# Kernel tuning notes

Measured on AMD Instinct MI355X. Metric: run time of the kernel, lower is better.

## Reference

```python
import jax, jax.numpy as jnp
import numpy as np

B, N, D = 32, 512, 256          # batch, instances, node_input_dim
M_DIM = 64                       # metric embedding dim
HID = 256                        # hidden_dim
COUNTS_PATTERN = [8, 16, 32, 72] # ragged per-instance metric counts (avg 32)


def _build_segments():
    counts = np.tile(np.array(COUNTS_PATTERN, dtype=np.int64), N // len(COUNTS_PATTERN))
    # metric_to_instance[t] = index of instance owning metric row t (contiguous ragged segments)
    return jnp.asarray(np.repeat(np.arange(N, dtype=np.int64), counts))


def setup_inputs() -> dict:
    key = jax.random.key(0)
    ks = jax.random.split(key, 8)
    metric_to_instance = _build_segments()
    T = int(metric_to_instance.shape[0])  # total_metrics = 16384
    h_instances = jax.random.normal(ks[0], (B, N, D), dtype=jnp.float32)
    metric_embeddings = jax.random.normal(ks[1], (B, T, M_DIM), dtype=jnp.float32)
    s = 0.02
    W1 = jax.random.normal(ks[2], (D + M_DIM, HID), dtype=jnp.float32) * s
    b1 = jnp.zeros((HID,), dtype=jnp.float32)
    W2 = jax.random.normal(ks[3], (HID, HID // 2), dtype=jnp.float32) * s
    b2 = jnp.zeros((HID // 2,), dtype=jnp.float32)
    W3 = jax.random.normal(ks[4], (HID // 2, 1), dtype=jnp.float32) * s
    b3 = jnp.zeros((1,), dtype=jnp.float32)
    return {
        "h_instances": h_instances,
        "metric_embeddings": metric_embeddings,
        "metric_to_instance": metric_to_instance,
        "W1": W1, "b1": b1, "W2": W2, "b2": b2, "W3": W3, "b3": b3,
    }


def reference(h_instances, metric_embeddings, metric_to_instance, W1, b1, W2, b2, W3, b3):
    # Gather each metric row's owning instance feature: [B, T, D]
    inst = jnp.take(h_instances, metric_to_instance, axis=1)
    # Concat with metric embedding -> [B, T, D + M_DIM]
    x = jnp.concatenate([inst, metric_embeddings], axis=-1)
    # metric_predictor MLP (Dropout is eval-mode identity in torch forward at inference)
    h = jax.nn.relu(jnp.einsum("btk,kh->bth", x, W1) + b1)
    h = jax.nn.relu(jnp.einsum("bth,hm->btm", h, W2) + b2)
    out = jnp.einsum("btm,mo->bto", h, W3) + b3  # [B, T, 1]
    return out[..., 0]  # [B, total_metrics]
```

## Files before the change

### kernel.cpp

```cpp
#include <hip/hip_runtime.h>

typedef _Float16 f16;
typedef f16  f16x2 __attribute__((ext_vector_type(2)));
typedef f16  f16x8 __attribute__((ext_vector_type(8)));
typedef float f32x16 __attribute__((ext_vector_type(16)));
typedef unsigned int u32;

#define MFMA32 __builtin_amdgcn_mfma_f32_32x32x16_f16

static __device__ __forceinline__ f16x8 cvt8(float4 a, float4 b) {
    f16x8 v;
    v[0]=(f16)a.x; v[1]=(f16)a.y; v[2]=(f16)a.z; v[3]=(f16)a.w;
    v[4]=(f16)b.x; v[5]=(f16)b.y; v[6]=(f16)b.z; v[7]=(f16)b.w;
    return v;
}
static __device__ __forceinline__ u32 pack2(float a, float b) {
    f16x2 p; p[0]=(f16)a; p[1]=(f16)b;
    return __builtin_bit_cast(u32, p);
}
static __device__ __forceinline__ u32 pk_add(u32 a, u32 b) {
    u32 d; asm("v_pk_add_f16 %0, %1, %2" : "=v"(d) : "v"(a), "v"(b)); return d;
}
static __device__ __forceinline__ u32 pk_relu(u32 a) {
    u32 d; asm("v_pk_max_f16 %0, %1, 0" : "=v"(d) : "v"(a)); return d;
}

__global__ __launch_bounds__(256) void prepack(
    const float* __restrict__ W1, const float* __restrict__ W2,
    f16* __restrict__ pa, f16* __restrict__ pb, f16* __restrict__ pc)
{
    const int idx = blockIdx.x * 256 + threadIdx.x;
    int rel, fid, mt, ks;
    const int lane = (idx >> 3) & 63;
    const int j    = idx & 7;
    const int g8   = ((lane >> 5) << 3) + j;
    const int ln   = lane & 31;
    if (idx < 65536) {
        rel = idx; fid = rel >> 9; mt = fid >> 4; ks = fid & 15;
        int k = 16 * ks + g8, col = 32 * mt + ln;
        pa[rel] = (f16)W1[k * 256 + col];
    } else if (idx < 81920) {
        rel = idx - 65536; fid = rel >> 9; mt = fid >> 2; ks = fid & 3;
        int k = 16 * ks + g8, col = 32 * mt + ln;
        pb[rel] = (f16)W1[(256 + k) * 256 + col];
    } else {
        rel = idx - 81920; fid = rel >> 9; mt = fid >> 4; ks = fid & 15;
        int k = 16 * ks + g8, col = 32 * mt + ln;
        pc[rel] = (f16)W2[k * 128 + col];
    }
}

__global__ __launch_bounds__(256) void ainit(
    const float* __restrict__ H,
    const f16x8* __restrict__ pW1a,
    const float* __restrict__ B1,
    f16* __restrict__ Af)
{
    const int tid = threadIdx.x, wid = tid >> 6, lane = tid & 63;
    const int g = lane >> 5, ln = lane & 31;
    const long ir = (long)blockIdx.x * 32 + ln;

    const float4* h4 = (const float4*)(H + ir * 256);
    f16x8 hf[16];
    #pragma unroll
    for (int ks = 0; ks < 16; ++ks)
        hf[ks] = cvt8(h4[4 * ks + 2 * g], h4[4 * ks + 2 * g + 1]);

    const float4* b14 = (const float4*)B1;
    #pragma unroll
    for (int mi = 0; mi < 2; ++mi) {
        const int mt = wid * 2 + mi;
        f32x16 acc;
        #pragma unroll
        for (int q = 0; q < 4; ++q) {
            float4 bv = b14[8 * mt + 2 * q + g];
            acc[4*q+0] = bv.x; acc[4*q+1] = bv.y; acc[4*q+2] = bv.z; acc[4*q+3] = bv.w;
        }
        #pragma unroll
        for (int ks = 0; ks < 16; ++ks)
            acc = MFMA32(pW1a[(mt * 16 + ks) * 64 + lane], hf[ks], acc, 0, 0, 0);
        #pragma unroll
        for (int q = 0; q < 4; ++q) {
            uint2 w;
            w.x = pack2(acc[4*q+0], acc[4*q+1]);
            w.y = pack2(acc[4*q+2], acc[4*q+3]);
            ((uint2*)Af)[ir * 64 + g * 32 + mt * 4 + q] = w;
        }
    }
}

__global__ __launch_bounds__(768, 3) void fused_mlp(
    const float* __restrict__ ME,
    const int*   __restrict__ SEG,
    const f16*   __restrict__ Af,
    const f16x8* __restrict__ pW1b,
    const f16x8* __restrict__ pW2,
    const float* __restrict__ B2,
    const float* __restrict__ W3,
    const float* __restrict__ B3,
    float* __restrict__ OUT)
{
    __shared__ f16x8 sW1b[2048];
    __shared__ f16x8 sW2[4096];
    const int tid = threadIdx.x, wid = tid >> 6, lane = tid & 63;
    const int g = lane >> 5, ln = lane & 31;

    for (int i = tid; i < 2048; i += 768) sW1b[i] = pW1b[i];
    for (int i = tid; i < 4096; i += 768) sW2[i]  = pW2[i];
    __syncthreads();

    const int bswz  = ((int)blockIdx.x & 7) * 32 + ((int)blockIdx.x >> 3);
    const int gwave = bswz * 12 + wid;

    const uint4* AB = (const uint4*)Af;
    const float4* b24 = (const float4*)B2;
    const float4* w34 = (const float4*)W3;
    const float  b3v  = B3[0];

    int tile = gwave;
    int ar_cur = ((tile >> 9) << 9) + SEG[((tile & 511) << 5) + ln];
    uint4 Av[4];
    #pragma unroll
    for (int u = 0; u < 4; ++u) Av[u] = AB[(long)ar_cur * 32 + g * 16 + u];

    while (true) {
        const int next = tile + 3072;
        int ar_nxt = ar_cur;
        if (next < 16384)
            ar_nxt = ((next >> 9) << 9) + SEG[((next & 511) << 5) + ln];

        const long row_base = (long)tile << 5;

        const float4* mb = (const float4*)(ME + (row_base + ln) * 64);
        float4 m0 = mb[2*g],     m1 = mb[2*g + 1];
        float4 m2_ = mb[4 + 2*g], m3 = mb[4 + 2*g + 1];
        float4 m4 = mb[8 + 2*g], m5 = mb[8 + 2*g + 1];
        float4 m6 = mb[12 + 2*g], m7 = mb[12 + 2*g + 1];
        f16x8 mef[4];
        mef[0] = cvt8(m0, m1); mef[1] = cvt8(m2_, m3);
        mef[2] = cvt8(m4, m5); mef[3] = cvt8(m6, m7);

        f32x16 acc2[4];
        #pragma unroll
        for (int m2 = 0; m2 < 4; ++m2)
            #pragma unroll
            for (int i = 0; i < 16; ++i) acc2[m2][i] = 0.f;

        #pragma unroll
        for (int mt = 0; mt < 8; ++mt) {
            const int sl = (mt & 1) * 2;
            const uint4 a0 = Av[sl], a1 = Av[sl + 1];
            {
                const int pos = mt + 2;
                if (pos < 8) {
                    Av[sl]     = AB[(long)ar_cur * 32 + g * 16 + 2*pos];
                    Av[sl + 1] = AB[(long)ar_cur * 32 + g * 16 + 2*pos + 1];
                } else if (next < 16384) {
                    const int mtn = pos - 8;
                    Av[sl]     = AB[(long)ar_nxt * 32 + g * 16 + 2*mtn];
                    Av[sl + 1] = AB[(long)ar_nxt * 32 + g * 16 + 2*mtn + 1];
                }
            }

            f32x16 acc;
            #pragma unroll
            for (int i = 0; i < 16; ++i) acc[i] = 0.f;
            #pragma unroll
            for (int s = 0; s < 4; ++s)
                acc = MFMA32(sW1b[(mt * 4 + s) * 64 + lane], mef[s], acc, 0, 0, 0);

            u32 hpt[8];
            hpt[0] = pk_relu(pk_add(pack2(acc[0],  acc[1]),  a0.x));
            hpt[1] = pk_relu(pk_add(pack2(acc[2],  acc[3]),  a0.y));
            hpt[2] = pk_relu(pk_add(pack2(acc[4],  acc[5]),  a0.z));
            hpt[3] = pk_relu(pk_add(pack2(acc[6],  acc[7]),  a0.w));
            hpt[4] = pk_relu(pk_add(pack2(acc[8],  acc[9]),  a1.x));
            hpt[5] = pk_relu(pk_add(pack2(acc[10], acc[11]), a1.y));
            hpt[6] = pk_relu(pk_add(pack2(acc[12], acc[13]), a1.z));
            hpt[7] = pk_relu(pk_add(pack2(acc[14], acc[15]), a1.w));

            #pragma unroll
            for (int tt = 0; tt < 2; ++tt) {
                u32 w0 = hpt[4*tt+0], w1 = hpt[4*tt+1];
                u32 w2 = hpt[4*tt+2], w3 = hpt[4*tt+3];
                asm("v_permlane32_swap_b32 %0, %1" : "+v"(w0), "+v"(w2));
                asm("v_permlane32_swap_b32 %0, %1" : "+v"(w1), "+v"(w3));
                int wv[4] = {(int)w0, (int)w1, (int)w2, (int)w3};
                f16x8 bf;
                __builtin_memcpy(&bf, wv, 16);
                const int ks2 = 2 * mt + tt;
                __builtin_amdgcn_s_setprio(1);
                #pragma unroll
                for (int m2 = 0; m2 < 4; ++m2)
                    acc2[m2] = MFMA32(sW2[(m2 * 16 + ks2) * 64 + lane], bf, acc2[m2], 0, 0, 0);
                __builtin_amdgcn_s_setprio(0);
            }
        }

        float sum = 0.f;
        #pragma unroll
        for (int m2 = 0; m2 < 4; ++m2)
            #pragma unroll
            for (int q = 0; q < 4; ++q) {
                float4 bb = b24[8*m2 + 2*q + g];
                float4 ww = w34[8*m2 + 2*q + g];
                sum += fmaxf(acc2[m2][4*q+0] + bb.x, 0.f) * ww.x
                     + fmaxf(acc2[m2][4*q+1] + bb.y, 0.f) * ww.y
                     + fmaxf(acc2[m2][4*q+2] + bb.z, 0.f) * ww.z
                     + fmaxf(acc2[m2][4*q+3] + bb.w, 0.f) * ww.w;
            }
        sum += __shfl_xor(sum, 32, 64);
        if (lane < 32) OUT[row_base + ln] = sum + b3v;

        if (next >= 16384) break;
        tile = next;
        ar_cur = ar_nxt;
    }
}

extern "C" void kernel_launch(void* const* d_in, const int* in_sizes, int n_in,
                              void* d_out, int out_size, void* d_ws, size_t ws_size,
                              hipStream_t stream) {
    const float* h_inst = (const float*)d_in[0];
    const float* me     = (const float*)d_in[1];
    const int*   seg    = (const int*)d_in[2];
    const float* W1     = (const float*)d_in[3];
    const float* b1     = (const float*)d_in[4];
    const float* W2     = (const float*)d_in[5];
    const float* b2     = (const float*)d_in[6];
    const float* W3     = (const float*)d_in[7];
    const float* b3     = (const float*)d_in[8];
    float* out = (float*)d_out;

    char* ws = (char*)d_ws;
    f16* Af   = (f16*)ws;
    f16* pW1a = (f16*)(ws + 8388608);
    f16* pW1b = (f16*)(ws + 8388608 + 131072);
    f16* pW2  = (f16*)(ws + 8388608 + 131072 + 32768);

    prepack<<<448, 256, 0, stream>>>(W1, W2, pW1a, pW1b, pW2);
    ainit<<<512, 256, 0, stream>>>(h_inst, (const f16x8*)pW1a, b1, Af);
    fused_mlp<<<256, 768, 0, stream>>>(me, seg, Af, (const f16x8*)pW1b,
                                       (const f16x8*)pW2, b2, W3, b3, out);
}
```

Baseline: 94.97 us.

## Replace static tile striding with atomic work-stealing counter in fused MLP

Each wave now claims its next 32-row tile through a global atomic counter, which prepack resets, instead of walking a fixed swizzled stride of 3072 tiles. This is meant to even out load imbalance across waves and CUs. The cross-tile prefetch of the next tile's A rows is dropped: A loads now start at the top of each tile, and only the segment index is prefetched. In exchange the kernel pays one atomic per tile per wave and exposes more latency on the A loads.

Measured after the change: 258.7 us. 2.72x slower.

```diff
diff --git a/kernel.cpp b/kernel.cpp
--- a/kernel.cpp
+++ b/kernel.cpp
@@ -27,8 +27,10 @@
 
 __global__ __launch_bounds__(256) void prepack(
     const float* __restrict__ W1, const float* __restrict__ W2,
-    f16* __restrict__ pa, f16* __restrict__ pb, f16* __restrict__ pc)
+    f16* __restrict__ pa, f16* __restrict__ pb, f16* __restrict__ pc,
+    int* __restrict__ ctr)
 {
+    if (blockIdx.x == 0 && threadIdx.x == 0) *ctr = 0;
     const int idx = blockIdx.x * 256 + threadIdx.x;
     int rel, fid, mt, ks;
     const int lane = (idx >> 3) & 63;
@@ -98,47 +100,51 @@
     const float* __restrict__ B2,
     const float* __restrict__ W3,
     const float* __restrict__ B3,
+    int* __restrict__ ctr,
     float* __restrict__ OUT)
 {
     __shared__ f16x8 sW1b[2048];
     __shared__ f16x8 sW2[4096];
-    const int tid = threadIdx.x, wid = tid >> 6, lane = tid & 63;
+    const int tid = threadIdx.x, lane = tid & 63;
     const int g = lane >> 5, ln = lane & 31;
 
     for (int i = tid; i < 2048; i += 768) sW1b[i] = pW1b[i];
     for (int i = tid; i < 4096; i += 768) sW2[i]  = pW2[i];
     __syncthreads();
-
-    const int bswz  = ((int)blockIdx.x & 7) * 32 + ((int)blockIdx.x >> 3);
-    const int gwave = bswz * 12 + wid;
 
     const uint4* AB = (const uint4*)Af;
     const float4* b24 = (const float4*)B2;
     const float4* w34 = (const float4*)W3;
     const float  b3v  = B3[0];
 
-    int tile = gwave;
-    int ar_cur = ((tile >> 9) << 9) + SEG[((tile & 511) << 5) + ln];
-    uint4 Av[4];
-    #pragma unroll
-    for (int u = 0; u < 4; ++u) Av[u] = AB[(long)ar_cur * 32 + g * 16 + u];
+    int cur;
+    if (lane == 0) cur = atomicAdd(ctr, 1);
+    cur = __builtin_amdgcn_readfirstlane(cur);
+    if (cur >= 16384) return;
+    int sv_cur = SEG[((cur & 511) << 5) + ln];
 
     while (true) {
-        const int next = tile + 3072;
-        int ar_nxt = ar_cur;
-        if (next < 16384)
-            ar_nxt = ((next >> 9) << 9) + SEG[((next & 511) << 5) + ln];
-
-        const long row_base = (long)tile << 5;
+        int nxt;
+        if (lane == 0) nxt = atomicAdd(ctr, 1);
+        nxt = __builtin_amdgcn_readfirstlane(nxt);
+        int sv_nxt = 0;
+        if (nxt < 16384) sv_nxt = SEG[((nxt & 511) << 5) + ln];
+
+        const long row_base = (long)cur << 5;
+        const int  ar = ((cur >> 9) << 9) + sv_cur;
+
+        uint4 Av[4];
+        #pragma unroll
+        for (int u = 0; u < 4; ++u) Av[u] = AB[(long)ar * 32 + g * 16 + u];
 
         const float4* mb = (const float4*)(ME + (row_base + ln) * 64);
-        float4 m0 = mb[2*g],     m1 = mb[2*g + 1];
+        float4 m0 = mb[2*g],      m1 = mb[2*g + 1];
         float4 m2_ = mb[4 + 2*g], m3 = mb[4 + 2*g + 1];
-        float4 m4 = mb[8 + 2*g], m5 = mb[8 + 2*g + 1];
+        float4 m4 = mb[8 + 2*g],  m5 = mb[8 + 2*g + 1];
         float4 m6 = mb[12 + 2*g], m7 = mb[12 + 2*g + 1];
         f16x8 mef[4];
-        mef[0] = cvt8(m0, m1); mef[1] = cvt8(m2_, m3);
-        mef[2] = cvt8(m4, m5); mef[3] = cvt8(m6, m7);
+        mef[0] = cvt8(m0, m1);  mef[1] = cvt8(m2_, m3);
+        mef[2] = cvt8(m4, m5);  mef[3] = cvt8(m6, m7);
 
         f32x16 acc2[4];
         #pragma unroll
@@ -153,12 +159,8 @@
             {
                 const int pos = mt + 2;
                 if (pos < 8) {
-                    Av[sl]     = AB[(long)ar_cur * 32 + g * 16 + 2*pos];
-                    Av[sl + 1] = AB[(long)ar_cur * 32 + g * 16 + 2*pos + 1];
-                } else if (next < 16384) {
-                    const int mtn = pos - 8;
-                    Av[sl]     = AB[(long)ar_nxt * 32 + g * 16 + 2*mtn];
-                    Av[sl + 1] = AB[(long)ar_nxt * 32 + g * 16 + 2*mtn + 1];
+                    Av[sl]     = AB[(long)ar * 32 + g * 16 + 2*pos];
+                    Av[sl + 1] = AB[(long)ar * 32 + g * 16 + 2*pos + 1];
                 }
             }
 
@@ -212,9 +214,9 @@
         sum += __shfl_xor(sum, 32, 64);
         if (lane < 32) OUT[row_base + ln] = sum + b3v;
 
-        if (next >= 16384) break;
-        tile = next;
-        ar_cur = ar_nxt;
+        if (nxt >= 16384) break;
+        cur = nxt;
+        sv_cur = sv_nxt;
     }
 }
 
@@ -237,9 +239,10 @@
     f16* pW1a = (f16*)(ws + 8388608);
     f16* pW1b = (f16*)(ws + 8388608 + 131072);
     f16* pW2  = (f16*)(ws + 8388608 + 131072 + 32768);
-
-    prepack<<<448, 256, 0, stream>>>(W1, W2, pW1a, pW1b, pW2);
+    int* ctr  = (int*)(ws + 9437184);
+
+    prepack<<<448, 256, 0, stream>>>(W1, W2, pW1a, pW1b, pW2, ctr);
     ainit<<<512, 256, 0, stream>>>(h_inst, (const f16x8*)pW1a, b1, Af);
     fused_mlp<<<256, 768, 0, stream>>>(me, seg, Af, (const f16x8*)pW1b,
-                                       (const f16x8*)pW2, b2, W3, b3, out);
-}
+                                       (const f16x8*)pW2, b2, W3, b3, ctr, out);
+}
```
